# Performance work log

Measured on AMD Instinct MI355X. Metric: run time of the kernel, lower is better.

## Reference

```python
import jax, jax.numpy as jnp
import numpy as np
from jax import lax

B, N, C = 4, 16384, 384  # C = 2*dim
DIM = C // 2
HH = WW = 128


def setup_inputs() -> dict:
    key = jax.random.key(0)
    ks = jax.random.split(key, 5)
    x = jax.random.normal(ks[0], (B, N, C), dtype=jnp.float32)
    conv_w = jax.random.normal(ks[1], (DIM, DIM, 4, 4), dtype=jnp.float32) * (1.0 / np.sqrt(DIM * 16))
    conv_b = jax.random.normal(ks[2], (DIM,), dtype=jnp.float32) * 0.02
    ln_w = jnp.ones((C,), dtype=jnp.float32)
    ln_b = jnp.zeros((C,), dtype=jnp.float32)
    proj_w = jax.random.normal(ks[3], (C, C), dtype=jnp.float32) * (1.0 / np.sqrt(C))
    proj_b = jax.random.normal(ks[4], (C,), dtype=jnp.float32) * 0.02
    return {"x": x, "conv_w": conv_w, "conv_b": conv_b, "ln_w": ln_w,
            "ln_b": ln_b, "proj_w": proj_w, "proj_b": proj_b, "H": HH, "W": WW}


def _csb_forward(x, conv_w, conv_b, ln_w, ln_b, proj_w, proj_b, H, W):
    Bb, Nn, Cc = x.shape
    d = Cc // 2
    x1 = x[..., :d]   # [B, N, d]
    x2 = x[..., d:]   # [B, N, d]

    # --- SpatialCorrection ---
    img = jnp.transpose(x2, (0, 2, 1)).reshape(Bb, d, H, W)  # NCHW
    y = lax.conv_general_dilated(img, conv_w, window_strides=(4, 4),
                                 padding='VALID',
                                 dimension_numbers=('NCHW', 'OIHW', 'NCHW'))
    y = y + conv_b[None, :, None, None]
    x2c = y.reshape(Bb, d, Nn // 16)                          # [B, d, M]
    gate = jax.nn.sigmoid(jnp.einsum('bnd,bdm->bnm', x1, x2c))  # [B, N, M]
    sp = jnp.einsum('bnm,bdm->bnd', gate, x2c)                 # [B, N, d]

    # --- ChannelCorrection ---
    att = jax.nn.softmax(jnp.einsum('bnd,bne->bde', x1, x2), axis=-2)  # [B, d, d], softmax over dim=-2
    ch = jnp.einsum('bnd,bde->bne', x2, att)                   # [B, N, d]

    # --- concat + LN + proj ---
    cat = jnp.concatenate([sp, ch], axis=-1)                   # [B, N, 2d]
    mu = jnp.mean(cat, axis=-1, keepdims=True)
    var = jnp.mean(jnp.square(cat - mu), axis=-1, keepdims=True)
    ln = (cat - mu) * lax.rsqrt(var + 1e-5) * ln_w + ln_b
    out = jnp.einsum('bnc,oc->bno', ln, proj_w) + proj_b
    return jnp.transpose(out, (0, 2, 1))                       # [B, 2d, N]


def reference(x, conv_w, conv_b, ln_w, ln_b, proj_w, proj_b, H, W):
    return _csb_forward(x, conv_w, conv_b, ln_w, ln_b, proj_w, proj_b, H, W)
```

## Files before the change

kernel.cpp:

```cpp
#include <hip/hip_runtime.h>
#include <hip/hip_bf16.h>

#define BB 4
#define NN 16384
#define CC 384
#define DD 192
#define MM 1024

typedef __attribute__((ext_vector_type(8))) short short8;
typedef __attribute__((ext_vector_type(4))) float f32x4;
typedef unsigned short u16;

__device__ __forceinline__ float4 ld4(const float* p) { return *reinterpret_cast<const float4*>(p); }

__device__ __forceinline__ u16 bf16r(float f) {
    unsigned int u = __float_as_uint(f);
    return (u16)((u + 0x7FFFu + ((u >> 16) & 1u)) >> 16);
}
__device__ __forceinline__ unsigned int pk2(float a, float b) {
    return (unsigned int)bf16r(a) | ((unsigned int)bf16r(b) << 16);
}
__device__ __forceinline__ unsigned int pk2c(float a, float b) {
    __hip_bfloat162 h = __float22bfloat162_rn(make_float2(a, b));
    union { __hip_bfloat162 h2; unsigned int u; } c; c.h2 = h; return c.u;
}
__device__ __forceinline__ short8 as_s8(uint4 v) {
    union { uint4 u; short8 s; } x; x.u = v; return x.s;
}
__device__ __forceinline__ f32x4 mfma16(short8 a, short8 b, f32x4 c) {
    return __builtin_amdgcn_mfma_f32_16x16x32_bf16(a, b, c, 0, 0, 0);
}
__device__ __forceinline__ void gload16(const void* g, void* l) {
    __builtin_amdgcn_global_load_lds(
        (const __attribute__((address_space(1))) void*)g,
        (__attribute__((address_space(3))) void*)l, 16, 0, 0);
}

__global__ __launch_bounds__(256) void k_prep(const float* __restrict__ pw, u16* __restrict__ pwb)
{
    int i = blockIdx.x * 256 + threadIdx.x;
    float4 v = ld4(&pw[i * 4]);
    uint2 o; o.x = pk2(v.x, v.y); o.y = pk2(v.z, v.w);
    reinterpret_cast<uint2*>(pwb)[i] = o;
}

__global__ __launch_bounds__(256) void k_prepw(const float* __restrict__ cw, u16* __restrict__ cwb)
{
    int idx = blockIdx.x * 256 + threadIdx.x;
    int k8 = idx / 192, o = idx % 192;
    int px = k8 / 24;
    int i0 = (k8 % 24) * 8;
    float f[8];
    #pragma unroll
    for (int e = 0; e < 8; ++e) f[e] = cw[(size_t)(o * 192 + i0 + e) * 16 + px];
    uint4 v = make_uint4(pk2(f[0], f[1]), pk2(f[2], f[3]), pk2(f[4], f[5]), pk2(f[6], f[7]));
    reinterpret_cast<uint4*>(cwb)[idx] = v;
}

__global__ __launch_bounds__(256) void k_conv(const float* __restrict__ x,
                                              const u16* __restrict__ cwb,
                                              float* __restrict__ Cp2)
{
    const int bid = blockIdx.x;
    const int s = bid >> 8, pt = bid & 255;
    const int b = pt >> 6;
    const int m0 = (pt & 63) * 16;
    const int P0 = pt * 16;
    const int t = threadIdx.x;
    const int l = t & 63, w = t >> 6;
    const int l15 = l & 15, l4 = l >> 4;
    const int o0 = w * 48;

    const int m = m0 + l15;
    const int ph = m >> 5, pw_ = m & 31;
    const float* xp = x + ((size_t)(b * NN) + ph * 512 + pw_ * 4) * CC + DD;

    f32x4 acc[3];
    #pragma unroll
    for (int ft = 0; ft < 3; ++ft) acc[ft] = (f32x4){0.f, 0.f, 0.f, 0.f};

    for (int kt = 0; kt < 48; ++kt) {
        const int px = s * 8 + kt / 6;
        const int i0 = (kt % 6) * 32;
        const int kh = px >> 2, kw = px & 3;
        const float* src = xp + (size_t)(kh * 128 + kw) * CC + i0 + l4 * 8;
        float4 v0 = ld4(src), v1 = ld4(src + 4);
        short8 av = as_s8(make_uint4(pk2(v0.x, v0.y), pk2(v0.z, v0.w), pk2(v1.x, v1.y), pk2(v1.z, v1.w)));
        const int k8g = px * 24 + (kt % 6) * 4 + l4;
        #pragma unroll
        for (int ft = 0; ft < 3; ++ft) {
            int o = o0 + ft * 16 + l15;
            short8 bv = as_s8(*reinterpret_cast<const uint4*>(cwb + (size_t)(k8g * 192 + o) * 8));
            acc[ft] = mfma16(av, bv, acc[ft]);
        }
    }
    #pragma unroll
    for (int ft = 0; ft < 3; ++ft)
        #pragma unroll
        for (int i = 0; i < 4; ++i)
            Cp2[(size_t)(s * 4096 + P0 + l4 * 4 + i) * 192 + o0 + ft * 16 + l15] = acc[ft][i];
}

__global__ __launch_bounds__(256) void k_convred(const float* __restrict__ Cp2,
                                                 const float* __restrict__ cb,
                                                 u16* __restrict__ x2cT,
                                                 u16* __restrict__ x2cM)
{
    __shared__ u16 T[64 * 194];
    const int bid = blockIdx.x;
    const int b = bid >> 4, mc = bid & 15;
    const int P0 = b * 1024 + mc * 64;
    const int t = threadIdx.x;
    #pragma unroll
    for (int j = 0; j < 12; ++j) {
        int idx = j * 256 + t;
        int row = idx / 48, c4 = idx % 48;
        float4 v0 = ld4(&Cp2[(size_t)(P0 + row) * 192 + c4 * 4]);
        float4 v1 = ld4(&Cp2[(size_t)(4096 + P0 + row) * 192 + c4 * 4]);
        float4 bb = ld4(&cb[c4 * 4]);
        float r0 = v0.x + v1.x + bb.x, r1 = v0.y + v1.y + bb.y;
        float r2 = v0.z + v1.z + bb.z, r3 = v0.w + v1.w + bb.w;
        u16 h0 = bf16r(r0), h1 = bf16r(r1), h2 = bf16r(r2), h3 = bf16r(r3);
        uint2 ov; ov.x = (unsigned int)h0 | ((unsigned int)h1 << 16);
        ov.y = (unsigned int)h2 | ((unsigned int)h3 << 16);
        *reinterpret_cast<uint2*>(x2cT + (size_t)(P0 + row) * 192 + c4 * 4) = ov;
        T[row * 194 + c4 * 4 + 0] = h0; T[row * 194 + c4 * 4 + 1] = h1;
        T[row * 194 + c4 * 4 + 2] = h2; T[row * 194 + c4 * 4 + 3] = h3;
    }
    __syncthreads();
    #pragma unroll
    for (int j = 0; j < 6; ++j) {
        int u = j * 256 + t;
        int o = u >> 3, m8 = (u & 7) * 8;
        unsigned int pk[4];
        #pragma unroll
        for (int q = 0; q < 4; ++q) {
            u16 a = T[(m8 + q * 2) * 194 + o];
            u16 c = T[(m8 + q * 2 + 1) * 194 + o];
            pk[q] = (unsigned int)a | ((unsigned int)c << 16);
        }
        *reinterpret_cast<uint4*>(x2cM + ((size_t)(b * DD + o) * MM) + mc * 64 + m8) =
            make_uint4(pk[0], pk[1], pk[2], pk[3]);
    }
}

__global__ __launch_bounds__(512) void k_S(const float* __restrict__ x, float* __restrict__ Sp,
                                           int KS, int nkt)
{
    __shared__ char LS[384 * 128];
    const int bid = blockIdx.x;
    const int b = bid / KS, ks = bid % KS;
    const int n0 = ks * (NN / KS);
    const int t = threadIdx.x;
    const int l = t & 63, w = t >> 6;
    const int rg = w >> 2, cs = w & 3;
    const int l15 = l & 15, l4 = l >> 4, key = (l15 & 7) << 4;

    const int c0 = (t & 127) * 3;
    const int krow = t >> 7;

    f32x4 acc[6][3];
    #pragma unroll
    for (int dt = 0; dt < 6; ++dt)
        #pragma unroll
        for (int et = 0; et < 3; ++et) acc[dt][et] = (f32x4){0.f, 0.f, 0.f, 0.f};

    for (int kt = 0; kt < nkt; ++kt) {
        __syncthreads();
        #pragma unroll
        for (int i = 0; i < 8; ++i) {
            int k = i * 4 + krow;
            const float* src = &x[(size_t)(b * NN + n0 + kt * 32 + k) * CC + c0];
            #pragma unroll
            for (int j = 0; j < 3; ++j) {
                int c = c0 + j;
                float v = src[j];
                u16 hi = bf16r(v);
                float hif = __uint_as_float(((unsigned int)hi) << 16);
                u16 lo = bf16r(v - hif);
                int base = c * 128;
                int ck = (c & 7) << 4;
                *reinterpret_cast<u16*>(LS + base + ((k * 2) ^ ck)) = hi;
                *reinterpret_cast<u16*>(LS + base + ((64 + k * 2) ^ ck)) = lo;
            }
        }
        __syncthreads();
        short8 bf[3][2];
        #pragma unroll
        for (int et = 0; et < 3; ++et) {
            int c = 192 + cs * 48 + et * 16 + l15;
            #pragma unroll
            for (int hl = 0; hl < 2; ++hl)
                bf[et][hl] = *reinterpret_cast<const short8*>(LS + c * 128 + ((hl * 64 + l4 * 16) ^ key));
        }
        #pragma unroll
        for (int dt = 0; dt < 6; ++dt) {
            int c = rg * 96 + dt * 16 + l15;
            short8 ah = *reinterpret_cast<const short8*>(LS + c * 128 + ((l4 * 16) ^ key));
            short8 al = *reinterpret_cast<const short8*>(LS + c * 128 + ((64 + l4 * 16) ^ key));
            #pragma unroll
            for (int et = 0; et < 3; ++et) {
                acc[dt][et] = mfma16(ah, bf[et][0], acc[dt][et]);
                acc[dt][et] = mfma16(ah, bf[et][1], acc[dt][et]);
                acc[dt][et] = mfma16(al, bf[et][0], acc[dt][et]);
            }
        }
    }
    float* dst = Sp + (size_t)(ks * BB + b) * 36864;
    #pragma unroll
    for (int dt = 0; dt < 6; ++dt)
        #pragma unroll
        for (int et = 0; et < 3; ++et) {
            int e = cs * 48 + et * 16 + l15;
            #pragma unroll
            for (int i = 0; i < 4; ++i) {
                int d = rg * 96 + dt * 16 + l4 * 4 + i;
                dst[d * 192 + e] = acc[dt][et][i];
            }
        }
}

__global__ __launch_bounds__(256) void k_sreduce(const float* __restrict__ Sp, float* __restrict__ S, int KS)
{
    int idx = blockIdx.x * 256 + threadIdx.x;
    int b = idx / 36864, de = idx % 36864;
    float s = 0.f;
    for (int p = 0; p < KS; ++p) s += Sp[(size_t)(p * BB + b) * 36864 + de];
    S[(size_t)b * 36864 + de] = s;
}

__global__ __launch_bounds__(64) void k_softmax(const float* __restrict__ S, u16* __restrict__ attT)
{
    const int bid = blockIdx.x;
    const int b = bid / 192, e = bid % 192;
    const int l = threadIdx.x;
    const float* Sb = S + (size_t)b * 36864 + e;
    float v0 = Sb[(size_t)(l * 3 + 0) * 192];
    float v1 = Sb[(size_t)(l * 3 + 1) * 192];
    float v2 = Sb[(size_t)(l * 3 + 2) * 192];
    float m = fmaxf(fmaxf(v0, v1), v2);
    #pragma unroll
    for (int s = 1; s < 64; s <<= 1) m = fmaxf(m, __shfl_xor(m, s, 64));
    v0 = __expf(v0 - m); v1 = __expf(v1 - m); v2 = __expf(v2 - m);
    float sum = v0 + v1 + v2;
    #pragma unroll
    for (int s = 1; s < 64; s <<= 1) sum += __shfl_xor(sum, s, 64);
    float inv = __fdividef(1.f, sum);
    u16* dst = attT + (size_t)b * 36864 + (size_t)e * 192 + l * 3;
    dst[0] = bf16r(v0 * inv); dst[1] = bf16r(v1 * inv); dst[2] = bf16r(v2 * inv);
}

#define KF_PW  50176
#define KF_GT  73728

__global__ __launch_bounds__(256, 2) void k_fused2(
    const float* __restrict__ x, const u16* __restrict__ x2cT,
    const u16* __restrict__ attT,
    const float* __restrict__ lnw, const float* __restrict__ lnb,
    const u16* __restrict__ pwb, const float* __restrict__ pb,
    float* __restrict__ out)
{
    __shared__ alignas(16) char LB[77824];
    const int t = threadIdx.x;
    const int l = t & 63, w = t >> 6;
    const int rg = w >> 1, cs = w & 1;
    const int b = blockIdx.x >> 8;
    const int n0 = (blockIdx.x & 255) << 6;
    const int l15 = l & 15, l4 = l >> 4, key = (l15 & 7) << 4;
    const int key3 = (l15 & 3) << 4;
    const size_t xrow0 = (size_t)(b * NN + n0) * CC;
    const char* cbase = (const char*)x2cT;

    int goff[6], gmul[6];
    #pragma unroll
    for (int it = 0; it < 6; ++it) {
        int q = it * 4096 + t * 16;
        if (q < 12288) {
            int m = q / 384, c = q % 384;
            goff[it] = b * 393216 + m * 384 + (c ^ ((m & 7) << 4));
            gmul[it] = 12288;
        } else {
            int qp = q - 12288;
            int r = qp >> 7, o = qp & 127;
            int op = o ^ ((r & 7) << 4);
            int d = r * 2 + (op >> 6);
            int m = (op & 63) >> 1;
            goff[it] = 1572864 + b * 393216 + d * 2048 + m * 2;
            gmul[it] = 64;
        }
    }

    short8 ax1[2][6];
    #pragma unroll
    for (int rt = 0; rt < 2; ++rt) {
        int row = rg * 32 + rt * 16 + l15;
        const float* src = &x[xrow0 + (size_t)row * CC + l4 * 8];
        #pragma unroll
        for (int k = 0; k < 6; ++k) {
            float4 v0 = ld4(src + k * 32), v1 = ld4(src + k * 32 + 4);
            ax1[rt][k] = as_s8(make_uint4(pk2(v0.x, v0.y), pk2(v0.z, v0.w), pk2(v1.x, v1.y), pk2(v1.z, v1.w)));
        }
    }

    char* bA = LB;
    char* bB = LB + 24576;
    char* bC = LB + 49152;
    #pragma unroll
    for (int it = 0; it < 6; ++it)
        gload16(cbase + goff[it], bA + it * 4096 + w * 1024);
    #pragma unroll
    for (int it = 0; it < 6; ++it)
        gload16(cbase + goff[it] + gmul[it], bB + it * 4096 + w * 1024);

    f32x4 spa[2][6];
    #pragma unroll
    for (int rt = 0; rt < 2; ++rt)
        #pragma unroll
        for (int nt = 0; nt < 6; ++nt) spa[rt][nt] = (f32x4){0.f, 0.f, 0.f, 0.f};

    char* GTb = LB + KF_GT;

    for (int mc = 0; mc < 32; ++mc) {
        if (mc < 31) asm volatile("s_waitcnt vmcnt(6)" ::: "memory");
        else         asm volatile("s_waitcnt vmcnt(0)" ::: "memory");
        __builtin_amdgcn_s_barrier();
        __builtin_amdgcn_sched_barrier(0);
        if (mc + 2 < 32) {
            #pragma unroll
            for (int it = 0; it < 6; ++it)
                gload16(cbase + goff[it] + (mc + 2) * gmul[it], bC + it * 4096 + w * 1024);
        }
        const char* bufCT = bA;
        const char* bufCM = bA + 12288;

        short8 bv[6];
        #pragma unroll
        for (int nt = 0; nt < 6; ++nt) {
            const int d = cs * 96 + nt * 16 + l15;
            const int rr = d >> 1;
            bv[nt] = *reinterpret_cast<const short8*>(
                bufCM + rr * 128 + ((((d & 1) * 64) + l4 * 16) ^ ((rr & 7) << 4)));
        }

        f32x4 cp[2];
        cp[0] = (f32x4){0.f, 0.f, 0.f, 0.f};
        cp[1] = (f32x4){0.f, 0.f, 0.f, 0.f};
        #pragma unroll
        for (int kblk = 0; kblk < 6; ++kblk) {
            short8 a_ = *reinterpret_cast<const short8*>(
                bufCT + (cs * 16 + l15) * 384 + ((kblk * 64 + l4 * 16) ^ key));
            cp[0] = mfma16(a_, ax1[0][kblk], cp[0]);
            cp[1] = mfma16(a_, ax1[1][kblk], cp[1]);
        }
        #pragma unroll
        for (int rt = 0; rt < 2; ++rt) {
            float g0 = __fdividef(1.f, 1.f + __expf(-cp[rt][0]));
            float g1 = __fdividef(1.f, 1.f + __expf(-cp[rt][1]));
            float g2 = __fdividef(1.f, 1.f + __expf(-cp[rt][2]));
            float g3 = __fdividef(1.f, 1.f + __expf(-cp[rt][3]));
            uint2 gv; gv.x = pk2c(g0, g1); gv.y = pk2c(g2, g3);
            *reinterpret_cast<uint2*>(GTb + (rg * 32 + rt * 16 + l15) * 64 +
                ((cs * 32 + l4 * 8) ^ key3)) = gv;
        }
        asm volatile("s_waitcnt lgkmcnt(0)" ::: "memory");
        __builtin_amdgcn_s_barrier();
        __builtin_amdgcn_sched_barrier(0);
        short8 ag[2];
        #pragma unroll
        for (int rt = 0; rt < 2; ++rt)
            ag[rt] = *reinterpret_cast<const short8*>(
                GTb + (rg * 32 + rt * 16 + l15) * 64 + ((l4 * 16) ^ key3));
        #pragma unroll
        for (int nt = 0; nt < 6; ++nt) {
            spa[0][nt] = mfma16(ag[0], bv[nt], spa[0][nt]);
            spa[1][nt] = mfma16(ag[1], bv[nt], spa[1][nt]);
        }
        char* tmp = bA; bA = bB; bB = bC; bC = tmp;
    }

    short8 ax2[2][6];
    #pragma unroll
    for (int rt = 0; rt < 2; ++rt) {
        int row = rg * 32 + rt * 16 + l15;
        const float* src = &x[xrow0 + (size_t)row * CC + DD + l4 * 8];
        #pragma unroll
        for (int k = 0; k < 6; ++k) {
            float4 v0 = ld4(src + k * 32), v1 = ld4(src + k * 32 + 4);
            ax2[rt][k] = as_s8(make_uint4(pk2(v0.x, v0.y), pk2(v0.z, v0.w), pk2(v1.x, v1.y), pk2(v1.z, v1.w)));
        }
    }
    f32x4 cha[2][6];
    #pragma unroll
    for (int rt = 0; rt < 2; ++rt)
        #pragma unroll
        for (int nt = 0; nt < 6; ++nt) cha[rt][nt] = (f32x4){0.f, 0.f, 0.f, 0.f};
    const u16* atb = attT + (size_t)b * 36864;
    #pragma unroll
    for (int nt = 0; nt < 6; ++nt) {
        int e = cs * 96 + nt * 16 + l15;
        #pragma unroll
        for (int k = 0; k < 6; ++k) {
            short8 bve = *reinterpret_cast<const short8*>(atb + (size_t)e * 192 + k * 32 + l4 * 8);
            cha[0][nt] = mfma16(ax2[0][k], bve, cha[0][nt]);
            cha[1][nt] = mfma16(ax2[1][k], bve, cha[1][nt]);
        }
    }
    __syncthreads();

    #pragma unroll
    for (int rt = 0; rt < 2; ++rt)
        #pragma unroll
        for (int nt = 0; nt < 6; ++nt) {
            int d = cs * 96 + nt * 16 + l15;
            #pragma unroll
            for (int i = 0; i < 4; ++i) {
                int row = rg * 32 + rt * 16 + l4 * 4 + i;
                *reinterpret_cast<u16*>(LB + (row * 392 + d) * 2) = bf16r(spa[rt][nt][i]);
                *reinterpret_cast<u16*>(LB + (row * 392 + DD + d) * 2) = bf16r(cha[rt][nt][i]);
            }
        }
    __syncthreads();

    {
        const int rowL = t >> 2, q = t & 3;
        char* lbase = LB + (rowL * 392 + q * 96) * 2;
        float s = 0.f, ss = 0.f;
        #pragma unroll
        for (int u = 0; u < 12; ++u) {
            uint4 pv = *reinterpret_cast<const uint4*>(lbase + u * 16);
            const unsigned int* pu = &pv.x;
            #pragma unroll
            for (int h = 0; h < 4; ++h) {
                float f0 = __uint_as_float(pu[h] << 16);
                float f1 = __uint_as_float(pu[h] & 0xFFFF0000u);
                s += f0 + f1; ss += f0 * f0 + f1 * f1;
            }
        }
        s += __shfl_xor(s, 1, 4);  s += __shfl_xor(s, 2, 4);
        ss += __shfl_xor(ss, 1, 4); ss += __shfl_xor(ss, 2, 4);
        float mu = s * (1.f / 384.f);
        float var = ss * (1.f / 384.f) - mu * mu;
        float rs = rsqrtf(var + 1e-5f);
        const int c0 = q * 96;
        #pragma unroll
        for (int u = 0; u < 12; ++u) {
            uint4 pv = *reinterpret_cast<const uint4*>(lbase + u * 16);
            const unsigned int* pu = &pv.x;
            float4 w0 = ld4(&lnw[c0 + u * 8]), w1 = ld4(&lnw[c0 + u * 8 + 4]);
            float4 b0 = ld4(&lnb[c0 + u * 8]), b1 = ld4(&lnb[c0 + u * 8 + 4]);
            float f[8];
            #pragma unroll
            for (int h = 0; h < 4; ++h) {
                f[2 * h]     = __uint_as_float(pu[h] << 16);
                f[2 * h + 1] = __uint_as_float(pu[h] & 0xFFFF0000u);
            }
            f[0] = (f[0] - mu) * rs * w0.x + b0.x; f[1] = (f[1] - mu) * rs * w0.y + b0.y;
            f[2] = (f[2] - mu) * rs * w0.z + b0.z; f[3] = (f[3] - mu) * rs * w0.w + b0.w;
            f[4] = (f[4] - mu) * rs * w1.x + b1.x; f[5] = (f[5] - mu) * rs * w1.y + b1.y;
            f[6] = (f[6] - mu) * rs * w1.z + b1.z; f[7] = (f[7] - mu) * rs * w1.w + b1.w;
            *reinterpret_cast<uint4*>(lbase + u * 16) =
                make_uint4(pk2c(f[0], f[1]), pk2c(f[2], f[3]), pk2c(f[4], f[5]), pk2c(f[6], f[7]));
        }
    }

    f32x4 pacc[2][12];
    #pragma unroll
    for (int rt = 0; rt < 2; ++rt)
        #pragma unroll
        for (int nt = 0; nt < 12; ++nt) pacc[rt][nt] = (f32x4){0.f, 0.f, 0.f, 0.f};
    for (int kt = 0; kt < 12; ++kt) {
        __syncthreads();
        #pragma unroll
        for (int j = 0; j < 6; ++j) {
            int u = j * 256 + t;
            int o = u >> 2, c8 = (u & 3) * 8;
            uint4 pv = *reinterpret_cast<const uint4*>(pwb + (size_t)o * CC + kt * 32 + c8);
            *reinterpret_cast<uint4*>(LB + KF_PW + (((o * 32 + c8) * 2) ^ ((o & 7) << 4))) = pv;
        }
        __syncthreads();
        short8 av[2];
        #pragma unroll
        for (int rt = 0; rt < 2; ++rt) {
            int row = rg * 32 + rt * 16 + l15;
            av[rt] = *reinterpret_cast<const short8*>(LB + (row * 392 + kt * 32 + l4 * 8) * 2);
        }
        #pragma unroll
        for (int nt = 0; nt < 12; ++nt) {
            int o = cs * 192 + nt * 16 + l15;
            short8 bvp = *reinterpret_cast<const short8*>(
                LB + KF_PW + (((o * 32 + l4 * 8) * 2) ^ ((o & 7) << 4)));
            pacc[0][nt] = mfma16(av[0], bvp, pacc[0][nt]);
            pacc[1][nt] = mfma16(av[1], bvp, pacc[1][nt]);
        }
    }
    __syncthreads();

    float* T = reinterpret_cast<float*>(LB + KF_PW);
    for (int os = 0; os < 6; ++os) {
        if (cs == (os >= 3 ? 1 : 0)) {
            const int nt0 = (os % 3) * 4;
            #pragma unroll
            for (int nt = 0; nt < 4; ++nt) {
                int o_l = nt * 16 + l15;
                float bias = pb[os * 64 + o_l];
                #pragma unroll
                for (int rt = 0; rt < 2; ++rt)
                    #pragma unroll
                    for (int i = 0; i < 4; ++i)
                        T[o_l * 68 + rg * 32 + rt * 16 + l4 * 4 + i] = pacc[rt][nt0 + nt][i] + bias;
            }
        }
        __syncthreads();
        {
            const int o_l = t >> 2, nq = t & 3;
            const size_t gbase = (size_t)(b * CC + os * 64 + o_l) * NN + n0 + nq * 16;
            #pragma unroll
            for (int j = 0; j < 4; ++j) {
                float4 v = *reinterpret_cast<const float4*>(&T[o_l * 68 + nq * 16 + j * 4]);
                *reinterpret_cast<float4*>(&out[gbase + j * 4]) = v;
            }
        }
        __syncthreads();
    }
}

extern "C" void kernel_launch(void* const* d_in, const int* in_sizes, int n_in,
                              void* d_out, int out_size, void* d_ws, size_t ws_size,
                              hipStream_t stream)
{
    (void)in_sizes; (void)n_in; (void)out_size;
    const float* x   = (const float*)d_in[0];
    const float* cw  = (const float*)d_in[1];
    const float* cb  = (const float*)d_in[2];
    const float* lnw = (const float*)d_in[3];
    const float* lnb = (const float*)d_in[4];
    const float* pwm = (const float*)d_in[5];
    const float* pbv = (const float*)d_in[6];
    float* out = (float*)d_out;
    char* w0 = (char*)d_ws;

    u16* x2cT = (u16*)(w0);
    u16* x2cM = (u16*)(w0 + 1572864);
    u16* attT = (u16*)(w0 + 3145728);
    u16* pwb  = (u16*)(w0 + 3440640);
    u16* cwb  = (u16*)(w0 + 3735552);
    float* Cp2 = (float*)(w0 + 4915200);
    float* Sp  = (float*)(w0 + 11206656);
    float* Sf  = (float*)(w0 + 30081024);

    int KS = 32;
    if (ws_size >= (size_t)68419584) {
        KS = 64;
        Sp = (float*)(w0 + 30670848);
    }
    const int nkt = (NN / KS) / 32;

    hipLaunchKernelGGL(k_prep,    dim3(144),      dim3(256), 0, stream, pwm, pwb);
    hipLaunchKernelGGL(k_prepw,   dim3(288),      dim3(256), 0, stream, cw, cwb);
    hipLaunchKernelGGL(k_conv,    dim3(512),      dim3(256), 0, stream, x, cwb, Cp2);
    hipLaunchKernelGGL(k_convred, dim3(64),       dim3(256), 0, stream, Cp2, cb, x2cT, x2cM);
    hipLaunchKernelGGL(k_S,       dim3(BB * KS),  dim3(512), 0, stream, x, Sp, KS, nkt);
    hipLaunchKernelGGL(k_sreduce, dim3(576),      dim3(256), 0, stream, Sp, Sf, KS);
    hipLaunchKernelGGL(k_softmax, dim3(BB * 192), dim3(64),  0, stream, Sf, attT);
    hipLaunchKernelGGL(k_fused2,  dim3(1024),     dim3(256), 0, stream,
                       x, x2cT, attT, lnw, lnb, pwb, pbv, out);
}
```

Baseline: 282.2 us.

## Shrink LDS footprint to raise occupancy: double-buffer gate loop, read proj weights from global

Cuts the shared-memory buffer from about 76KB to 52KB so three blocks can share a CU instead of two. The spatial-gate loop drops from a triple buffer with a two-ahead prefetch to a double buffer with a one-ahead prefetch and a full barrier each iteration. The projection GEMM no longer stages weight tiles in LDS and instead reads bf16 weights from global memory per wavefront, and the transpose staging buffer moves to offset zero. The shorter prefetch distance, extra barriers and uncoalesced global weight reads may offset the higher occupancy.

```diff
diff --git a/kernel.cpp b/kernel.cpp
--- a/kernel.cpp
+++ b/kernel.cpp
@@ -250,17 +250,16 @@
     dst[0] = bf16r(v0 * inv); dst[1] = bf16r(v1 * inv); dst[2] = bf16r(v2 * inv);
 }
 
-#define KF_PW  50176
-#define KF_GT  73728
-
-__global__ __launch_bounds__(256, 2) void k_fused2(
+#define KF_GT  49152
+
+__global__ __launch_bounds__(256, 3) void k_fused2(
     const float* __restrict__ x, const u16* __restrict__ x2cT,
     const u16* __restrict__ attT,
     const float* __restrict__ lnw, const float* __restrict__ lnb,
     const u16* __restrict__ pwb, const float* __restrict__ pb,
     float* __restrict__ out)
 {
-    __shared__ alignas(16) char LB[77824];
+    __shared__ alignas(16) char LB[53248];
     const int t = threadIdx.x;
     const int l = t & 63, w = t >> 6;
     const int rg = w >> 1, cs = w & 1;
@@ -302,15 +301,10 @@
         }
     }
 
-    char* bA = LB;
-    char* bB = LB + 24576;
-    char* bC = LB + 49152;
     #pragma unroll
     for (int it = 0; it < 6; ++it)
-        gload16(cbase + goff[it], bA + it * 4096 + w * 1024);
-    #pragma unroll
-    for (int it = 0; it < 6; ++it)
-        gload16(cbase + goff[it] + gmul[it], bB + it * 4096 + w * 1024);
+        gload16(cbase + goff[it], LB + it * 4096 + w * 1024);
+    __syncthreads();
 
     f32x4 spa[2][6];
     #pragma unroll
@@ -320,18 +314,17 @@
 
     char* GTb = LB + KF_GT;
 
+    int p = 0;
     for (int mc = 0; mc < 32; ++mc) {
-        if (mc < 31) asm volatile("s_waitcnt vmcnt(6)" ::: "memory");
-        else         asm volatile("s_waitcnt vmcnt(0)" ::: "memory");
-        __builtin_amdgcn_s_barrier();
-        __builtin_amdgcn_sched_barrier(0);
-        if (mc + 2 < 32) {
+        if (mc < 31) {
+            const int pn = p ^ 1;
             #pragma unroll
             for (int it = 0; it < 6; ++it)
-                gload16(cbase + goff[it] + (mc + 2) * gmul[it], bC + it * 4096 + w * 1024);
-        }
-        const char* bufCT = bA;
-        const char* bufCM = bA + 12288;
+                gload16(cbase + goff[it] + (mc + 1) * gmul[it],
+                        LB + pn * 24576 + it * 4096 + w * 1024);
+        }
+        const char* bufCT = LB + p * 24576;
+        const char* bufCM = bufCT + 12288;
 
         short8 bv[6];
         #pragma unroll
@@ -375,7 +368,8 @@
             spa[0][nt] = mfma16(ag[0], bv[nt], spa[0][nt]);
             spa[1][nt] = mfma16(ag[1], bv[nt], spa[1][nt]);
         }
-        char* tmp = bA; bA = bB; bB = bC; bC = tmp;
+        __syncthreads();
+        p ^= 1;
     }
 
     short8 ax2[2][6];
@@ -405,8 +399,6 @@
             cha[1][nt] = mfma16(ax2[1][k], bve, cha[1][nt]);
         }
     }
-    __syncthreads();
-
     #pragma unroll
     for (int rt = 0; rt < 2; ++rt)
         #pragma unroll
@@ -462,6 +454,7 @@
                 make_uint4(pk2c(f[0], f[1]), pk2c(f[2], f[3]), pk2c(f[4], f[5]), pk2c(f[6], f[7]));
         }
     }
+    __syncthreads();
 
     f32x4 pacc[2][12];
     #pragma unroll
@@ -469,33 +462,24 @@
         #pragma unroll
         for (int nt = 0; nt < 12; ++nt) pacc[rt][nt] = (f32x4){0.f, 0.f, 0.f, 0.f};
     for (int kt = 0; kt < 12; ++kt) {
-        __syncthreads();
-        #pragma unroll
-        for (int j = 0; j < 6; ++j) {
-            int u = j * 256 + t;
-            int o = u >> 2, c8 = (u & 3) * 8;
-            uint4 pv = *reinterpret_cast<const uint4*>(pwb + (size_t)o * CC + kt * 32 + c8);
-            *reinterpret_cast<uint4*>(LB + KF_PW + (((o * 32 + c8) * 2) ^ ((o & 7) << 4))) = pv;
-        }
-        __syncthreads();
         short8 av[2];
         #pragma unroll
         for (int rt = 0; rt < 2; ++rt) {
             int row = rg * 32 + rt * 16 + l15;
             av[rt] = *reinterpret_cast<const short8*>(LB + (row * 392 + kt * 32 + l4 * 8) * 2);
         }
+        const u16* pwk = pwb + kt * 32 + l4 * 8;
         #pragma unroll
         for (int nt = 0; nt < 12; ++nt) {
             int o = cs * 192 + nt * 16 + l15;
-            short8 bvp = *reinterpret_cast<const short8*>(
-                LB + KF_PW + (((o * 32 + l4 * 8) * 2) ^ ((o & 7) << 4)));
+            short8 bvp = as_s8(*reinterpret_cast<const uint4*>(pwk + (size_t)o * CC));
             pacc[0][nt] = mfma16(av[0], bvp, pacc[0][nt]);
             pacc[1][nt] = mfma16(av[1], bvp, pacc[1][nt]);
         }
     }
     __syncthreads();
 
-    float* T = reinterpret_cast<float*>(LB + KF_PW);
+    float* T = reinterpret_cast<float*>(LB);
     for (int os = 0; os < 6; ++os) {
         if (cs == (os >= 3 ? 1 : 0)) {
             const int nt0 = (os % 3) * 4;
```

New measurement: 341.1 us. 20.8% more time.
